# Kernel tuning notes

Hardware: AMD Instinct MI355X
Metric: run time of the kernel (lower is better)

Reference implementation:

```python
import jax, jax.numpy as jnp
import numpy as np
import math

N_EMBD = 1024
N_HEAD = 16
HEAD_DIM = N_EMBD // N_HEAD

def setup_inputs() -> dict:
    key = jax.random.key(0)
    k1, k2, k3, k4, k5 = jax.random.split(key, 5)
    s = 1.0 / math.sqrt(N_EMBD)
    x = jax.random.normal(k1, (4, 2048, N_EMBD), dtype=jnp.float32)
    W_qkv = jax.random.normal(k2, (N_EMBD, 3 * N_EMBD), dtype=jnp.float32) * s
    b_qkv = jnp.zeros((3 * N_EMBD,), dtype=jnp.float32)
    W_proj = jax.random.normal(k3, (N_EMBD, N_EMBD), dtype=jnp.float32) * s
    b_proj = jnp.zeros((N_EMBD,), dtype=jnp.float32)
    return {"x": x, "W_qkv": W_qkv, "b_qkv": b_qkv, "W_proj": W_proj, "b_proj": b_proj}

def reference(x, W_qkv, b_qkv, W_proj, b_proj):
    B, T, C = x.shape
    H, D = N_HEAD, HEAD_DIM
    qkv = x @ W_qkv + b_qkv                      # (B,T,3C)
    qkv = qkv.reshape(B, T, 3, H, D)
    q = jnp.transpose(qkv[:, :, 0], (0, 2, 1, 3))  # (B,H,T,D)
    k = jnp.transpose(qkv[:, :, 1], (0, 2, 1, 3))
    v = jnp.transpose(qkv[:, :, 2], (0, 2, 1, 3))
    scale = 1.0 / math.sqrt(D)
    att = jnp.einsum('bhtd,bhsd->bhts', q, k) * scale  # (B,H,T,T)
    causal = jnp.tril(jnp.ones((T, T), dtype=bool))
    att = jnp.where(causal[None, None], att, -jnp.inf)
    att = jax.nn.softmax(att, axis=-1)
    out = jnp.einsum('bhts,bhsd->bhtd', att, v)   # (B,H,T,D)
    out = jnp.transpose(out, (0, 2, 1, 3)).reshape(B, T, C)
    return out @ W_proj + b_proj
```

## Files before the change

kernel.cpp:

```cpp
#include <hip/hip_runtime.h>
#include <stdint.h>


typedef __attribute__((ext_vector_type(8))) __bf16 bf16x8_t;
typedef __attribute__((ext_vector_type(4))) float f32x4_t;
typedef __attribute__((ext_vector_type(16))) float f32x16_t;
typedef __attribute__((ext_vector_type(4))) unsigned short u16x4_t;
typedef __attribute__((ext_vector_type(4))) unsigned int u32x4_t;

static __device__ __forceinline__ unsigned short f2bf(float f) {
  union { float f; unsigned u; } c; c.f = f;
  unsigned r = c.u + 0x7FFFu + ((c.u >> 16) & 1u);
  return (unsigned short)(r >> 16);
}

static __device__ __forceinline__ unsigned cvt_pk_bf16(float lo, float hi) {
  unsigned r;
  asm volatile("v_cvt_pk_bf16_f32 %0, %1, %2" : "=v"(r) : "v"(lo), "v"(hi));
  return r;
}

static __device__ __forceinline__ void perm32swap(unsigned& a, unsigned& b) {
  asm volatile("v_permlane32_swap_b32 %0, %1" : "+v"(a), "+v"(b));
}

static __device__ __forceinline__ f32x16_t zero16() {
  f32x16_t v;
#pragma unroll
  for (int i = 0; i < 16; ++i) v[i] = 0.f;
  return v;
}

static __device__ __forceinline__ void gload16(const void* g, void* lds) {
  __builtin_amdgcn_global_load_lds(
      (const __attribute__((address_space(1))) unsigned int*)g,
      (__attribute__((address_space(3))) unsigned int*)(uint32_t)(uintptr_t)lds,
      16, 0, 0);
}

__global__ __launch_bounds__(256) void k_cast_bf16(const float* __restrict__ in,
                                                   unsigned short* __restrict__ out) {
  int i = blockIdx.x * 256 + threadIdx.x;
  float4 v = ((const float4*)in)[i];
  u16x4_t r = { f2bf(v.x), f2bf(v.y), f2bf(v.z), f2bf(v.w) };
  ((u16x4_t*)out)[i] = r;
}

__global__ __launch_bounds__(256) void k_transpose_cast(const float* __restrict__ W,
                                                        unsigned short* __restrict__ Wt,
                                                        int Kd, int Nd) {
  __shared__ float tile[32][33];
  int n0 = blockIdx.x * 32, k0 = blockIdx.y * 32;
  int tx = threadIdx.x, ty = threadIdx.y;
#pragma unroll
  for (int i = 0; i < 4; ++i)
    tile[ty + 8 * i][tx] = W[(size_t)(k0 + ty + 8 * i) * Nd + n0 + tx];
  __syncthreads();
#pragma unroll
  for (int i = 0; i < 4; ++i)
    Wt[(size_t)(n0 + ty + 8 * i) * Kd + k0 + tx] = f2bf(tile[tx][ty + 8 * i]);
}

static __device__ __forceinline__ void gemm128_core(
    const unsigned short* __restrict__ A, const unsigned short* __restrict__ Bt,
    int Kdim, int rowBase, int colBase,
    unsigned short* As, unsigned short* Bs, f32x4_t acc[4][4]) {
  const int tid = threadIdx.x;
  const int lane = tid & 63;
  const int wr = (tid >> 7) & 1;
  const int wc = (tid >> 6) & 1;
  const unsigned short* aSrc = A + (size_t)(rowBase + (tid >> 2)) * Kdim + (tid & 3) * 8;
  const unsigned short* bSrc = Bt + (size_t)(colBase + (tid >> 2)) * Kdim + (tid & 3) * 8;
  unsigned short* aDst0 = As + tid * 8;
  unsigned short* aDst1 = As + tid * 8 + 2048;
  unsigned short* bDst0 = Bs + tid * 8;
  unsigned short* bDst1 = Bs + tid * 8 + 2048;
  const int ar = wr * 64 + (lane & 15);
  const int br = wc * 64 + (lane & 15);
  const int kk = (lane >> 4) * 8;
  for (int k0 = 0; k0 < Kdim; k0 += 32) {
    gload16(aSrc + k0, aDst0);
    gload16(aSrc + k0 + 64 * Kdim, aDst1);
    gload16(bSrc + k0, bDst0);
    gload16(bSrc + k0 + 64 * Kdim, bDst1);
    __syncthreads();
    bf16x8_t af[4], bfr[4];
#pragma unroll
    for (int m = 0; m < 4; ++m) af[m] = *(const bf16x8_t*)&As[(ar + m * 16) * 32 + kk];
#pragma unroll
    for (int n = 0; n < 4; ++n) bfr[n] = *(const bf16x8_t*)&Bs[(br + n * 16) * 32 + kk];
#pragma unroll
    for (int m = 0; m < 4; ++m)
#pragma unroll
      for (int n = 0; n < 4; ++n)
        acc[m][n] = __builtin_amdgcn_mfma_f32_16x16x32_bf16(af[m], bfr[n], acc[m][n], 0, 0, 0);
    __syncthreads();
  }
}

__global__ __launch_bounds__(256) void k_gemm_qkv(
    const unsigned short* __restrict__ A, const unsigned short* __restrict__ Bt,
    const float* __restrict__ bias,
    unsigned short* __restrict__ Qo, unsigned short* __restrict__ Ko,
    unsigned short* __restrict__ Vo) {
  __shared__ alignas(16) unsigned short As[128 * 32];
  __shared__ alignas(16) unsigned short Bs[128 * 32];
  f32x4_t acc[4][4];
  f32x4_t z = {0.f, 0.f, 0.f, 0.f};
#pragma unroll
  for (int m = 0; m < 4; ++m)
#pragma unroll
    for (int n = 0; n < 4; ++n) acc[m][n] = z;
  gemm128_core(A, Bt, 1024, blockIdx.y * 128, blockIdx.x * 128, As, Bs, acc);
  const int tid = threadIdx.x, lane = tid & 63;
  const int wr = (tid >> 7) & 1, wc = (tid >> 6) & 1;
#pragma unroll
  for (int n = 0; n < 4; ++n) {
    int col = blockIdx.x * 128 + wc * 64 + n * 16 + (lane & 15);
    int which = col >> 10;
    int h = (col >> 6) & 15;
    int d = col & 63;
    float bv = bias[col];
#pragma unroll
    for (int m = 0; m < 4; ++m)
#pragma unroll
      for (int r = 0; r < 4; ++r) {
        int row = blockIdx.y * 128 + wr * 64 + m * 16 + ((lane >> 4) * 4) + r;
        int b = row >> 11, t = row & 2047;
        float val = acc[m][n][r] + bv;
        if (which == 0)
          Qo[(size_t)((b * 16 + h) * 2048 + t) * 64 + d] = f2bf(val * 0.18033688011112042f);
        else if (which == 1)
          Ko[(size_t)((b * 16 + h) * 2048 + t) * 64 + d] = f2bf(val);
        else
          Vo[(size_t)((b * 16 + h) * 64 + d) * 2048 + t] = f2bf(val);
      }
  }
}

__global__ __launch_bounds__(256) void k_gemm_proj(
    const unsigned short* __restrict__ A, const unsigned short* __restrict__ Bt,
    const float* __restrict__ bias, float* __restrict__ out) {
  __shared__ alignas(16) unsigned short As[128 * 32];
  __shared__ alignas(16) unsigned short Bs[128 * 32];
  f32x4_t acc[4][4];
  f32x4_t z = {0.f, 0.f, 0.f, 0.f};
#pragma unroll
  for (int m = 0; m < 4; ++m)
#pragma unroll
    for (int n = 0; n < 4; ++n) acc[m][n] = z;
  gemm128_core(A, Bt, 1024, blockIdx.y * 128, blockIdx.x * 128, As, Bs, acc);
  const int tid = threadIdx.x, lane = tid & 63;
  const int wr = (tid >> 7) & 1, wc = (tid >> 6) & 1;
#pragma unroll
  for (int n = 0; n < 4; ++n) {
    int col = blockIdx.x * 128 + wc * 64 + n * 16 + (lane & 15);
    float bv = bias[col];
#pragma unroll
    for (int m = 0; m < 4; ++m)
#pragma unroll
      for (int r = 0; r < 4; ++r) {
        int row = blockIdx.y * 128 + wr * 64 + m * 16 + ((lane >> 4) * 4) + r;
        out[(size_t)row * 1024 + col] = acc[m][n][r] + bv;
      }
  }
}

__global__ __launch_bounds__(256) void k_attn(const unsigned short* __restrict__ Q,
                                              const unsigned short* __restrict__ K,
                                              const unsigned short* __restrict__ Vt,
                                              unsigned short* __restrict__ O) {
  __shared__ alignas(16) unsigned short KT[2][4096];
  __shared__ alignas(16) unsigned short VT[2][4096];
  const int flat = blockIdx.x;
  const int bx = 15 - (flat >> 6);
  const int bh = flat & 63;
  const int tid = threadIdx.x;
  const int lane = tid & 63;
  const int w = tid >> 6;
  const int l31 = lane & 31;
  const int hi = lane >> 5;
  const int sw = l31 & 7;
  const unsigned short* Qh = Q + (size_t)bh * 2048 * 64;
  const unsigned short* Kh = K + (size_t)bh * 2048 * 64;
  const unsigned short* Vh = Vt + (size_t)bh * 64 * 2048;
  const int qrow = bx * 128 + w * 32;
  const int qg = qrow + l31;
  const int NT = 2 * bx + 2;

  bf16x8_t qf[4];
#pragma unroll
  for (int s = 0; s < 4; ++s)
    qf[s] = *(const bf16x8_t*)&Qh[(size_t)qg * 64 + s * 16 + hi * 8];

  f32x16_t ot0 = zero16(), ot1 = zero16();
  float m_r = -1e30f, l_r = 0.f;

  const int srow = tid >> 3;
  const int ssw = 8 * ((tid & 7) ^ (srow & 7));
  auto STAGE = [&](int t_, int buf_) {
#pragma unroll
    for (int i = 0; i < 2; ++i) {
      const int r_ = i * 32 + srow;
      gload16(Kh + (size_t)(t_ * 64 + r_) * 64 + ssw, &KT[buf_][i * 2048 + tid * 8]);
      gload16(Vh + (size_t)r_ * 2048 + t_ * 64 + ssw, &VT[buf_][i * 2048 + tid * 8]);
    }
  };

  STAGE(0, 0);
  __syncthreads();
  for (int t = 0; t < NT; ++t) {
    const int buf = t & 1;
    if (t + 1 < NT) STAGE(t + 1, buf ^ 1);
    if (t * 64 <= qrow + 31) {
      f32x16_t st[2];
#pragma unroll
      for (int tt = 0; tt < 2; ++tt) {
        st[tt] = zero16();
        const unsigned short* kr = &KT[buf][(tt * 32 + l31) * 64];
#pragma unroll
        for (int s = 0; s < 4; ++s) {
          bf16x8_t kf = *(const bf16x8_t*)&kr[((2 * s + hi) ^ sw) * 8];
          st[tt] = __builtin_amdgcn_mfma_f32_32x32x16_bf16(kf, qf[s], st[tt], 0, 0, 0);
        }
      }
      if (t * 64 + 63 > qrow) {
#pragma unroll
        for (int tt = 0; tt < 2; ++tt)
#pragma unroll
          for (int r = 0; r < 16; ++r) {
            int kv = t * 64 + tt * 32 + (r & 3) + 8 * (r >> 2) + 4 * hi;
            if (kv > qg) st[tt][r] = -1e30f;
          }
      }
      float mx = st[0][0];
#pragma unroll
      for (int tt = 0; tt < 2; ++tt)
#pragma unroll
        for (int r = 0; r < 16; ++r) mx = fmaxf(mx, st[tt][r]);
      mx = fmaxf(mx, __shfl_xor(mx, 32));
      float mnew = fmaxf(m_r, mx);
      float resc = __builtin_amdgcn_exp2f(m_r - mnew);
      float u = 0.f;
#pragma unroll
      for (int tt = 0; tt < 2; ++tt)
#pragma unroll
        for (int r = 0; r < 16; ++r) {
          float pv = __builtin_amdgcn_exp2f(st[tt][r] - mnew);
          st[tt][r] = pv;
          u += pv;
        }
      u += __shfl_xor(u, 32);
      l_r = l_r * resc + u;
      m_r = mnew;
      ot0 *= resc;
      ot1 *= resc;
#pragma unroll
      for (int tt = 0; tt < 2; ++tt) {
        unsigned W0 = cvt_pk_bf16(st[tt][0], st[tt][1]);
        unsigned W1 = cvt_pk_bf16(st[tt][2], st[tt][3]);
        unsigned W2 = cvt_pk_bf16(st[tt][4], st[tt][5]);
        unsigned W3 = cvt_pk_bf16(st[tt][6], st[tt][7]);
        unsigned W4 = cvt_pk_bf16(st[tt][8], st[tt][9]);
        unsigned W5 = cvt_pk_bf16(st[tt][10], st[tt][11]);
        unsigned W6 = cvt_pk_bf16(st[tt][12], st[tt][13]);
        unsigned W7 = cvt_pk_bf16(st[tt][14], st[tt][15]);
        perm32swap(W0, W2);
        perm32swap(W1, W3);
        perm32swap(W4, W6);
        perm32swap(W5, W7);
        u32x4_t fe = {W0, W1, W2, W3};
        u32x4_t fo = {W4, W5, W6, W7};
        bf16x8_t pe = __builtin_bit_cast(bf16x8_t, fe);
        bf16x8_t po = __builtin_bit_cast(bf16x8_t, fo);
        const unsigned short* vr0 = &VT[buf][l31 * 64];
        const unsigned short* vr1 = &VT[buf][(32 + l31) * 64];
        bf16x8_t ve0 = *(const bf16x8_t*)&vr0[((4 * tt + hi) ^ sw) * 8];
        bf16x8_t vo0 = *(const bf16x8_t*)&vr0[((4 * tt + 2 + hi) ^ sw) * 8];
        bf16x8_t ve1 = *(const bf16x8_t*)&vr1[((4 * tt + hi) ^ sw) * 8];
        bf16x8_t vo1 = *(const bf16x8_t*)&vr1[((4 * tt + 2 + hi) ^ sw) * 8];
        ot0 = __builtin_amdgcn_mfma_f32_32x32x16_bf16(ve0, pe, ot0, 0, 0, 0);
        ot0 = __builtin_amdgcn_mfma_f32_32x32x16_bf16(vo0, po, ot0, 0, 0, 0);
        ot1 = __builtin_amdgcn_mfma_f32_32x32x16_bf16(ve1, pe, ot1, 0, 0, 0);
        ot1 = __builtin_amdgcn_mfma_f32_32x32x16_bf16(vo1, po, ot1, 0, 0, 0);
      }
    }
    __syncthreads();
  }
  const float inv = 1.0f / l_r;
  const int b = bh >> 4, h = bh & 15;
  unsigned short* orow = O + (size_t)(b * 2048 + qg) * 1024 + h * 64;
#pragma unroll
  for (int m = 0; m < 4; ++m) {
    u16x4_t r0, r1;
#pragma unroll
    for (int j = 0; j < 4; ++j) {
      r0[j] = f2bf(ot0[4 * m + j] * inv);
      r1[j] = f2bf(ot1[4 * m + j] * inv);
    }
    *(u16x4_t*)&orow[8 * m + 4 * hi] = r0;
    *(u16x4_t*)&orow[32 + 8 * m + 4 * hi] = r1;
  }
}

extern "C" void kernel_launch(void* const* d_in, const int* in_sizes, int n_in,
                              void* d_out, int out_size, void* d_ws, size_t ws_size,
                              hipStream_t stream) {
  const float* x     = (const float*)d_in[0];
  const float* Wqkv  = (const float*)d_in[1];
  const float* bqkv  = (const float*)d_in[2];
  const float* Wproj = (const float*)d_in[3];
  const float* bproj = (const float*)d_in[4];
  float* out = (float*)d_out;

  char* ws = (char*)d_ws;
  unsigned short* xb     = (unsigned short*)(ws);
  unsigned short* wqkvT  = (unsigned short*)(ws + 16777216);
  unsigned short* wprojT = (unsigned short*)(ws + 23068672);
  unsigned short* Qb     = (unsigned short*)(ws + 25165824);
  unsigned short* Kb     = (unsigned short*)(ws + 41943040);
  unsigned short* Vb     = (unsigned short*)(ws + 58720256);
  unsigned short* Ob     = (unsigned short*)(ws + 75497472);

  k_cast_bf16<<<8192, 256, 0, stream>>>(x, xb);
  k_transpose_cast<<<dim3(96, 32), dim3(32, 8), 0, stream>>>(Wqkv, wqkvT, 1024, 3072);
  k_transpose_cast<<<dim3(32, 32), dim3(32, 8), 0, stream>>>(Wproj, wprojT, 1024, 1024);
  k_gemm_qkv<<<dim3(24, 64), 256, 0, stream>>>(xb, wqkvT, bqkv, Qb, Kb, Vb);
  k_attn<<<1024, 256, 0, stream>>>(Qb, Kb, Vb, Ob);
  k_gemm_proj<<<dim3(8, 64), 256, 0, stream>>>(Ob, wprojT, bproj, out);
}
```

Measured before the change: 288.7 us.

## Rework GEMM core with double-buffered 128x256 tiles, XOR-swizzled LDS, block swizzle

Replaces the 128x128, BK=32 single-buffered GEMM core with a 128x256, BK=64 tile run by 512 threads (8 waves). LDS is double-buffered so the next K tile's global-to-LDS loads overlap the current tile's MFMAs, and LDS chunks are XOR-swizzled to avoid bank conflicts. Block indices are remapped so neighbouring blocks share A/B tiles in L2. LDS use grows to 96KB per block, which limits occupancy, and the proj GEMM now launches only 256 blocks.

```diff
diff --git a/kernel.cpp b/kernel.cpp
--- a/kernel.cpp
+++ b/kernel.cpp
@@ -61,62 +61,85 @@
     Wt[(size_t)(n0 + ty + 8 * i) * Kd + k0 + tx] = f2bf(tile[tx][ty + 8 * i]);
 }
 
-static __device__ __forceinline__ void gemm128_core(
+static __device__ __forceinline__ void gemm_core(
     const unsigned short* __restrict__ A, const unsigned short* __restrict__ Bt,
-    int Kdim, int rowBase, int colBase,
-    unsigned short* As, unsigned short* Bs, f32x4_t acc[4][4]) {
+    int Kd, int bm0, int bn0,
+    unsigned short (*As)[128 * 64], unsigned short (*Bs)[256 * 64],
+    f32x4_t acc[4][4]) {
   const int tid = threadIdx.x;
   const int lane = tid & 63;
-  const int wr = (tid >> 7) & 1;
-  const int wc = (tid >> 6) & 1;
-  const unsigned short* aSrc = A + (size_t)(rowBase + (tid >> 2)) * Kdim + (tid & 3) * 8;
-  const unsigned short* bSrc = Bt + (size_t)(colBase + (tid >> 2)) * Kdim + (tid & 3) * 8;
-  unsigned short* aDst0 = As + tid * 8;
-  unsigned short* aDst1 = As + tid * 8 + 2048;
-  unsigned short* bDst0 = Bs + tid * 8;
-  unsigned short* bDst1 = Bs + tid * 8 + 2048;
-  const int ar = wr * 64 + (lane & 15);
-  const int br = wc * 64 + (lane & 15);
-  const int kk = (lane >> 4) * 8;
-  for (int k0 = 0; k0 < Kdim; k0 += 32) {
-    gload16(aSrc + k0, aDst0);
-    gload16(aSrc + k0 + 64 * Kdim, aDst1);
-    gload16(bSrc + k0, bDst0);
-    gload16(bSrc + k0 + 64 * Kdim, bDst1);
-    __syncthreads();
-    bf16x8_t af[4], bfr[4];
-#pragma unroll
-    for (int m = 0; m < 4; ++m) af[m] = *(const bf16x8_t*)&As[(ar + m * 16) * 32 + kk];
-#pragma unroll
-    for (int n = 0; n < 4; ++n) bfr[n] = *(const bf16x8_t*)&Bs[(br + n * 16) * 32 + kk];
-#pragma unroll
-    for (int m = 0; m < 4; ++m)
+  const int wid = tid >> 6;
+  const int wm = wid >> 2, wn = wid & 3;
+  const int l15 = lane & 15, lhi = lane >> 4;
+  const int trow = tid >> 3;
+  const int schunk = ((tid & 7) ^ (trow & 7)) * 8;
+  const unsigned short* aS = A + (size_t)(bm0 + trow) * Kd + schunk;
+  const unsigned short* bS = Bt + (size_t)(bn0 + trow) * Kd + schunk;
+  const int NK = Kd >> 6;
+
+  auto STAGE = [&](int kt, int sl) {
+    const size_t ko = (size_t)kt * 64;
+#pragma unroll
+    for (int j = 0; j < 2; ++j)
+      gload16(aS + ko + (size_t)(64 * j) * Kd, &As[sl][j * 4096 + tid * 8]);
+#pragma unroll
+    for (int j = 0; j < 4; ++j)
+      gload16(bS + ko + (size_t)(64 * j) * Kd, &Bs[sl][j * 4096 + tid * 8]);
+  };
+
+  STAGE(0, 0);
+  asm volatile("s_waitcnt vmcnt(0)" ::: "memory");
+  __builtin_amdgcn_s_barrier();
+  __builtin_amdgcn_sched_barrier(0);
+  for (int kt = 0; kt < NK; ++kt) {
+    const int sl = kt & 1;
+    if (kt + 1 < NK) STAGE(kt + 1, sl ^ 1);
+    __builtin_amdgcn_sched_barrier(0);
+#pragma unroll
+    for (int ks = 0; ks < 2; ++ks) {
+      const int ch = ((4 * ks + lhi) ^ (l15 & 7)) * 8;
+      bf16x8_t af[4], bfr[4];
+#pragma unroll
+      for (int m = 0; m < 4; ++m)
+        af[m] = *(const bf16x8_t*)&As[sl][(wm * 64 + m * 16 + l15) * 64 + ch];
 #pragma unroll
       for (int n = 0; n < 4; ++n)
-        acc[m][n] = __builtin_amdgcn_mfma_f32_16x16x32_bf16(af[m], bfr[n], acc[m][n], 0, 0, 0);
-    __syncthreads();
-  }
-}
-
-__global__ __launch_bounds__(256) void k_gemm_qkv(
+        bfr[n] = *(const bf16x8_t*)&Bs[sl][(wn * 64 + n * 16 + l15) * 64 + ch];
+#pragma unroll
+      for (int m = 0; m < 4; ++m)
+#pragma unroll
+        for (int n = 0; n < 4; ++n)
+          acc[m][n] = __builtin_amdgcn_mfma_f32_16x16x32_bf16(af[m], bfr[n], acc[m][n], 0, 0, 0);
+    }
+    asm volatile("s_waitcnt vmcnt(0)" ::: "memory");
+    __builtin_amdgcn_s_barrier();
+    __builtin_amdgcn_sched_barrier(0);
+  }
+}
+
+__global__ __launch_bounds__(512, 2) void k_gemm_qkv(
     const unsigned short* __restrict__ A, const unsigned short* __restrict__ Bt,
     const float* __restrict__ bias,
     unsigned short* __restrict__ Qo, unsigned short* __restrict__ Ko,
     unsigned short* __restrict__ Vo) {
-  __shared__ alignas(16) unsigned short As[128 * 32];
-  __shared__ alignas(16) unsigned short Bs[128 * 32];
+  __shared__ alignas(16) unsigned short As[2][128 * 64];
+  __shared__ alignas(16) unsigned short Bs[2][256 * 64];
+  const int orig = blockIdx.x;
+  const int swz = (orig & 7) * 96 + (orig >> 3);
+  const int by = swz / 12, bx = swz % 12;
   f32x4_t acc[4][4];
   f32x4_t z = {0.f, 0.f, 0.f, 0.f};
 #pragma unroll
   for (int m = 0; m < 4; ++m)
 #pragma unroll
     for (int n = 0; n < 4; ++n) acc[m][n] = z;
-  gemm128_core(A, Bt, 1024, blockIdx.y * 128, blockIdx.x * 128, As, Bs, acc);
+  gemm_core(A, Bt, 1024, by * 128, bx * 256, As, Bs, acc);
   const int tid = threadIdx.x, lane = tid & 63;
-  const int wr = (tid >> 7) & 1, wc = (tid >> 6) & 1;
+  const int wid = tid >> 6, wm = wid >> 2, wn = wid & 3;
+  const int l15 = lane & 15, lhi = lane >> 4;
 #pragma unroll
   for (int n = 0; n < 4; ++n) {
-    int col = blockIdx.x * 128 + wc * 64 + n * 16 + (lane & 15);
+    int col = bx * 256 + wn * 64 + n * 16 + l15;
     int which = col >> 10;
     int h = (col >> 6) & 15;
     int d = col & 63;
@@ -125,7 +148,7 @@
     for (int m = 0; m < 4; ++m)
 #pragma unroll
       for (int r = 0; r < 4; ++r) {
-        int row = blockIdx.y * 128 + wr * 64 + m * 16 + ((lane >> 4) * 4) + r;
+        int row = by * 128 + wm * 64 + m * 16 + lhi * 4 + r;
         int b = row >> 11, t = row & 2047;
         float val = acc[m][n][r] + bv;
         if (which == 0)
@@ -138,29 +161,33 @@
   }
 }
 
-__global__ __launch_bounds__(256) void k_gemm_proj(
+__global__ __launch_bounds__(512, 2) void k_gemm_proj(
     const unsigned short* __restrict__ A, const unsigned short* __restrict__ Bt,
     const float* __restrict__ bias, float* __restrict__ out) {
-  __shared__ alignas(16) unsigned short As[128 * 32];
-  __shared__ alignas(16) unsigned short Bs[128 * 32];
+  __shared__ alignas(16) unsigned short As[2][128 * 64];
+  __shared__ alignas(16) unsigned short Bs[2][256 * 64];
+  const int orig = blockIdx.x;
+  const int swz = (orig & 7) * 32 + (orig >> 3);
+  const int by = swz >> 2, bx = swz & 3;
   f32x4_t acc[4][4];
   f32x4_t z = {0.f, 0.f, 0.f, 0.f};
 #pragma unroll
   for (int m = 0; m < 4; ++m)
 #pragma unroll
     for (int n = 0; n < 4; ++n) acc[m][n] = z;
-  gemm128_core(A, Bt, 1024, blockIdx.y * 128, blockIdx.x * 128, As, Bs, acc);
+  gemm_core(A, Bt, 1024, by * 128, bx * 256, As, Bs, acc);
   const int tid = threadIdx.x, lane = tid & 63;
-  const int wr = (tid >> 7) & 1, wc = (tid >> 6) & 1;
+  const int wid = tid >> 6, wm = wid >> 2, wn = wid & 3;
+  const int l15 = lane & 15, lhi = lane >> 4;
 #pragma unroll
   for (int n = 0; n < 4; ++n) {
-    int col = blockIdx.x * 128 + wc * 64 + n * 16 + (lane & 15);
+    int col = bx * 256 + wn * 64 + n * 16 + l15;
     float bv = bias[col];
 #pragma unroll
     for (int m = 0; m < 4; ++m)
 #pragma unroll
       for (int r = 0; r < 4; ++r) {
-        int row = blockIdx.y * 128 + wr * 64 + m * 16 + ((lane >> 4) * 4) + r;
+        int row = by * 128 + wm * 64 + m * 16 + lhi * 4 + r;
         out[(size_t)row * 1024 + col] = acc[m][n][r] + bv;
       }
   }
@@ -325,7 +352,7 @@
   k_cast_bf16<<<8192, 256, 0, stream>>>(x, xb);
   k_transpose_cast<<<dim3(96, 32), dim3(32, 8), 0, stream>>>(Wqkv, wqkvT, 1024, 3072);
   k_transpose_cast<<<dim3(32, 32), dim3(32, 8), 0, stream>>>(Wproj, wprojT, 1024, 1024);
-  k_gemm_qkv<<<dim3(24, 64), 256, 0, stream>>>(xb, wqkvT, bqkv, Qb, Kb, Vb);
+  k_gemm_qkv<<<768, 512, 0, stream>>>(xb, wqkvT, bqkv, Qb, Kb, Vb);
   k_attn<<<1024, 256, 0, stream>>>(Qb, Kb, Vb, Ob);
-  k_gemm_proj<<<dim3(8, 64), 256, 0, stream>>>(Ob, wprojT, bproj, out);
-}
+  k_gemm_proj<<<256, 512, 0, stream>>>(Ob, wprojT, bproj, out);
+}
```

After: 271.4 us. 6.0% less time.
